# Performance work log

Hardware: AMD Instinct MI355X
Metric: run time of the kernel (lower is better)

## Reference

```python
import jax, jax.numpy as jnp
import numpy as np

B, S, A, E, H, V, P = 128, 256, 8, 300, 300, 50000, 3


def _gru(x, wih, whh, bih, bhh):
    """torch.nn.GRU (single layer, batch_first) with gate order r,z,n."""
    h0 = jnp.zeros((x.shape[0], whh.shape[1]), x.dtype)

    def step(h, xt):
        gi = xt @ wih.T + bih            # [B,3H]
        gh = h @ whh.T + bhh
        ir, iz, in_ = jnp.split(gi, 3, axis=-1)
        hr, hz, hn = jnp.split(gh, 3, axis=-1)
        r = jax.nn.sigmoid(ir + hr)
        z = jax.nn.sigmoid(iz + hz)
        n = jnp.tanh(in_ + r * hn)
        hnew = (1.0 - z) * n + z * h
        return hnew, hnew

    _, ys = jax.lax.scan(step, h0, jnp.swapaxes(x, 0, 1))  # scan over time
    return jnp.swapaxes(ys, 0, 1)                          # [B,S,H]


def setup_inputs() -> dict:
    key = jax.random.key(0)
    ks = jax.random.split(key, 16)
    rn = lambda k, shape, s=0.05: jax.random.normal(k, shape, jnp.float32) * s
    z = lambda *shape: jnp.zeros(shape, jnp.float32)
    return {
        "embed_table": rn(ks[0], (V, E), 1.0),
        "w1": rn(ks[1], (E, 3 * E)), "b1": z(E),
        "w2": rn(ks[2], (1, E)),
        "wm": rn(ks[3], (E, E)), "bm": z(E),
        "wd": rn(ks[4], (P, E)), "bd": z(P),
        "wih_l": rn(ks[5], (3 * H, E)), "whh_l": rn(ks[6], (3 * H, H)),
        "bih_l": z(3 * H), "bhh_l": z(3 * H),
        "wih_r": rn(ks[7], (3 * H, E)), "whh_r": rn(ks[8], (3 * H, H)),
        "bih_r": z(3 * H), "bhh_r": z(3 * H),
        "wml": rn(ks[9], (1, H)), "bml": z(1),
        "wmr": rn(ks[10], (1, H)), "bmr": z(1),
        # all token ids >= 1 so lengths are exactly the padded length (packing == identity)
        "text_raw_indices": jax.random.randint(ks[11], (B, S), 1, V),
        "aspect_indices": jax.random.randint(ks[12], (B, A), 1, V),
        "x_l": jax.random.randint(ks[13], (B, S), 1, V),
        "x_r": jax.random.randint(ks[14], (B, S), 1, V),
    }


def _forward(embed_table, w1, b1, w2, wm, bm, wd, bd,
             wih_l, whh_l, bih_l, bhh_l, wih_r, whh_r, bih_r, bhh_r,
             wml, bml, wmr, bmr, text, aspect, xl, xr):
    memory_len = jnp.sum(text != 0, -1)    # [B]
    aspect_len = jnp.sum(aspect != 0, -1)
    left_len = jnp.sum(xl != 0, -1)

    v_a = jnp.sum(embed_table[aspect], 1) / aspect_len[:, None].astype(jnp.float32)  # [B,E]
    memory = embed_table[text]             # [B,S,E]

    # ---- context attention (attention #1), fully vectorized ----
    ctx_l = _gru(embed_table[xl], wih_l, whh_l, bih_l, bhh_l)  # [B,S,H]
    ctx_r = _gru(embed_table[xr], wih_r, whh_r, bih_r, bhh_r)
    attn_l = jax.nn.sigmoid(jnp.einsum('bsh,h->bs', ctx_l, wml[0]) + bml[0]) + 0.5  # [B,S]
    attn_r = jax.nn.sigmoid(jnp.einsum('bsh,h->bs', ctx_r, wmr[0]) + bmr[0]) + 0.5

    idx = jnp.arange(S)[None, :]                      # [1,S]
    a_start = (left_len - aspect_len)[:, None]        # [B,1]
    a_end = left_len[:, None]
    # attn_r reversed over the first aspect_end positions: attn_rr[i,t] = attn_r[i, a_end-1-t]
    attn_rr = jnp.take_along_axis(attn_r, jnp.clip(a_end - 1 - idx, 0, S - 1), axis=1)
    # attn_l shifted by aspect_start: attn_ls[i,t] = attn_l[i, t - a_start]
    attn_ls = jnp.take_along_axis(attn_l, jnp.clip(idx - a_start, 0, S - 1), axis=1)
    w = jnp.where(idx < a_start, attn_rr,
                  jnp.where(idx < a_end, (attn_rr + attn_ls) * 0.5, attn_ls))
    w = jnp.where(idx < memory_len[:, None], w, 1.0)  # untouched past memory_len
    memory = memory * w[..., None]

    v_s = jnp.sum(memory, 1) / memory_len[:, None].astype(jnp.float32)  # [B,E]

    # ---- content attention (attention #2) ----
    feat = jnp.concatenate([memory,
                            jnp.broadcast_to(v_a[:, None, :], memory.shape),
                            jnp.broadcast_to(v_s[:, None, :], memory.shape)], -1)  # [B,S,3E]
    c = jnp.tanh(feat @ w1.T + b1) @ w2.T             # [B,S,1]
    alpha = jax.nn.softmax(c[..., 0], axis=1)         # [B,S]
    v_ts = jnp.einsum('bse,bs->be', memory, alpha)    # [B,E]

    v_ns = v_ts + v_s                                 # dropout is identity at eval
    v_ms = jnp.tanh(v_ns @ wm.T + bm)
    return jax.nn.softmax(v_ms @ wd.T + bd, axis=-1)  # [B,P]


def reference(embed_table, w1, b1, w2, wm, bm, wd, bd,
              wih_l, whh_l, bih_l, bhh_l, wih_r, whh_r, bih_r, bhh_r,
              wml, bml, wmr, bmr, text_raw_indices, aspect_indices, x_l, x_r):
    return _forward(embed_table, w1, b1, w2, wm, bm, wd, bd,
                    wih_l, whh_l, bih_l, bhh_l, wih_r, whh_r, bih_r, bhh_r,
                    wml, bml, wmr, bmr, text_raw_indices, aspect_indices, x_l, x_r)
```

## Files before the change

kernel.cpp:

```cpp
#include <hip/hip_runtime.h>
#include <hip/hip_bf16.h>
#include <math.h>

#define Bd 128
#define Sd 256
#define Ad 8
#define Ed 300
#define Hd 300
#define EP 320
#define Pd 3
#define UC 5
#define BG 8

typedef __attribute__((ext_vector_type(8))) short bfrag;
typedef __attribute__((ext_vector_type(4))) float f32x4;
typedef __attribute__((ext_vector_type(4))) int i32x4;

#define OFF_LENS   0u
#define OFF_FLAGS  4096u
#define OFF_VA     8192u
#define OFF_VS     172032u
#define OFF_U      335872u
#define OFF_ATTN   499712u
#define OFF_ALPHA  761856u
#define OFF_C      892928u
#define OFF_HF     1024000u
#define OFF_PART   1351680u
#define OFF_WF     11837440u
#define OFF_W1B    14295040u
#define OFF_XF     14499840u
#define OFF_MEMW   14499840u
#define WS_NEEDED  56442880u

__device__ __forceinline__ unsigned short f2bf(float f) {
    __hip_bfloat16 h = __float2bfloat16(f);
    return *reinterpret_cast<unsigned short*>(&h);
}
__device__ __forceinline__ float bf2f(unsigned short u) {
    __hip_bfloat16 h = *reinterpret_cast<__hip_bfloat16*>(&u);
    return __bfloat162float(h);
}
__device__ __forceinline__ float sigm(float x) {
    return __builtin_amdgcn_rcpf(1.f + __expf(-x));
}
__device__ __forceinline__ float fast_tanh(float x) {
    x = fminf(fmaxf(x, -15.f), 15.f);
    float e = __expf(2.f * x);
    return (e - 1.f) * __builtin_amdgcn_rcpf(e + 1.f);
}

__device__ __forceinline__ bfrag l2_load16b(const void* p) {
    bfrag v;
    asm volatile("global_load_dwordx4 %0, %1, off sc0"
                 : "=v"(v) : "v"(p) : "memory");
    return v;
}
__device__ __forceinline__ void l2_store16(void* p, i32x4 v) {
    asm volatile("global_store_dwordx4 %0, %1, off sc0"
                 :: "v"(p), "v"(v) : "memory");
}

__global__ void k_lengths(const int* __restrict__ text, const int* __restrict__ aspect,
                          const int* __restrict__ xl, int* __restrict__ lens) {
    int b = blockIdx.x;
    __shared__ int red[3];
    if (threadIdx.x < 3) red[threadIdx.x] = 0;
    __syncthreads();
    int t = threadIdx.x;
    if (t < Sd) {
        if (text[b*Sd + t] != 0) atomicAdd(&red[0], 1);
        if (xl[b*Sd + t]  != 0) atomicAdd(&red[2], 1);
    }
    if (t < Ad) { if (aspect[b*Ad + t] != 0) atomicAdd(&red[1], 1); }
    __syncthreads();
    if (t < 3) lens[b*4 + t] = red[t];
}

__global__ void k_va(const float* __restrict__ embed, const int* __restrict__ aspect,
                     const int* __restrict__ lens, float* __restrict__ va) {
    int b = blockIdx.x;
    __shared__ int aidx[Ad];
    if (threadIdx.x < Ad) aidx[threadIdx.x] = aspect[b*Ad + threadIdx.x];
    __syncthreads();
    float inv = 1.0f / (float)lens[b*4+1];
    for (int e = threadIdx.x; e < EP; e += blockDim.x) {
        float s = 0.f;
        if (e < Ed) {
            for (int a = 0; a < Ad; ++a) s += embed[(size_t)aidx[a]*Ed + e];
        }
        va[b*EP + e] = s * inv;
    }
}

__global__ void k_xf(const float* __restrict__ embed, const int* __restrict__ xl,
                     const int* __restrict__ xr, unsigned short* __restrict__ XF) {
    int side = blockIdx.x >> 8;
    int t = blockIdx.x & 255;
    const int* xs = side ? xr : xl;
    __shared__ int rows_s[Bd];
    if (threadIdx.x < Bd) rows_s[threadIdx.x] = xs[threadIdx.x*Sd + t];
    __syncthreads();
    unsigned short* dst = XF + ((size_t)(side*Sd + t))*40960;
    for (int idx = threadIdx.x; idx < 40960; idx += 256) {
        int bt = idx / 5120;
        int r1 = idx - bt*5120;
        int kt = r1 / 512;
        int r2 = r1 - kt*512;
        int lane = r2 >> 3, j = r2 & 7;
        int b = bt*16 + (lane & 15);
        int kk = kt*32 + (lane >> 4)*8 + j;
        float v = (kk < Ed) ? embed[(size_t)rows_s[b]*Ed + kk] : 0.f;
        dst[idx] = f2bf(v);
    }
}

__global__ void k_wfrag(const float* __restrict__ wih_l, const float* __restrict__ whh_l,
                        const float* __restrict__ wih_r, const float* __restrict__ whh_r,
                        unsigned short* __restrict__ WF) {
    int bid = blockIdx.x;
    int side = bid / 120;
    int r = bid - side*120;
    int mat = r / 60; r -= mat*60;
    int g = r / 20;
    int ut = r - g*20;
    const float* W = mat ? (side ? whh_r : whh_l) : (side ? wih_r : wih_l);
    unsigned short* dst = WF + (size_t)bid*5120;
    for (int idx = threadIdx.x; idx < 5120; idx += 256) {
        int kt = idx / 512;
        int r2 = idx - kt*512;
        int lane = r2 >> 3, j = r2 & 7;
        int unit = ut*16 + (lane & 15);
        int kk = kt*32 + (lane >> 4)*8 + j;
        float v = (unit < Hd && kk < Ed) ? W[(size_t)(g*Hd + unit)*Ed + kk] : 0.f;
        dst[idx] = f2bf(v);
    }
}

__global__ void k_w1conv(const float* __restrict__ w1, unsigned short* __restrict__ w1b) {
    int idx = blockIdx.x*256 + threadIdx.x;
    if (idx >= EP*EP) return;
    int e = idx / EP, k = idx - e*EP;
    float v = (e < Ed && k < Ed) ? w1[(size_t)e*900 + k] : 0.f;
    w1b[idx] = f2bf(v);
}

__global__ __launch_bounds__(256, 1) void k_gru(
        const unsigned short* __restrict__ WF,
        const unsigned short* __restrict__ XF,
        const float* __restrict__ bih_l, const float* __restrict__ bhh_l,
        const float* __restrict__ bih_r, const float* __restrict__ bhh_r,
        const float* __restrict__ wml, const float* __restrict__ wmr,
        unsigned short* __restrict__ HF,
        float* __restrict__ part, int* __restrict__ flags) {
    int bg = blockIdx.x & 7;
    int r8 = blockIdx.x >> 3;
    int side = r8 & 1;
    int uc = r8 >> 1;
    int tid = threadIdx.x;
    int w = tid >> 6, lane = tid & 63, ul = lane & 15, lq = lane >> 4;
    int utg = uc*4 + w;
    int u = utg*16 + ul;

    const float* bih = side ? bih_r : bih_l;
    const float* bhh = side ? bhh_r : bhh_l;
    const float* wmv = side ? wmr : wml;

    float bR=0.f, bZ=0.f, bNI=0.f, bNH=0.f, wml_r=0.f;
    if (u < Hd) {
        bR = bih[u] + bhh[u];
        bZ = bih[Hd+u] + bhh[Hd+u];
        bNI = bih[2*Hd+u];
        bNH = bhh[2*Hd+u];
        wml_r = wmv[u];
    }

    bfrag wI[3][10], wH[3][10];
    #pragma unroll
    for (int g = 0; g < 3; ++g) {
        const unsigned short* pI = WF + ((size_t)((side*2+0)*3+g)*20 + utg)*5120 + lane*8;
        const unsigned short* pH = WF + ((size_t)((side*2+1)*3+g)*20 + utg)*5120 + lane*8;
        #pragma unroll
        for (int kt = 0; kt < 10; ++kt) {
            wI[g][kt] = *(const bfrag*)(pI + kt*512);
            wH[g][kt] = *(const bfrag*)(pH + kt*512);
        }
    }

    __shared__ __align__(16) unsigned short hn_s[1024];
    int* flgL2 = flags + (side*8 + bg)*16;
    int* flgIC = flags + 512 + (side*8 + bg)*16;
    unsigned short* hfb = HF + (size_t)((side*8 + bg)*2)*5120;
    const unsigned short* xbase = XF + ((size_t)side*Sd*8 + bg)*5120 + lane*8;

    bfrag xA[10], xB[10];
    #pragma unroll
    for (int kt = 0; kt < 10; ++kt)
        xA[kt] = *(const bfrag*)(xbase + 0 + kt*512);

    float hreg[4] = {0.f,0.f,0.f,0.f};
    const f32x4 zero4 = {0.f,0.f,0.f,0.f};

#define GRU_STEP(T, XIN, XOUT) do {                                            \
    f32x4 aR = zero4, aZ = zero4, aNI = zero4, aNH = zero4;                    \
    _Pragma("unroll")                                                          \
    for (int kt = 0; kt < 10; ++kt) {                                          \
        aR  = __builtin_amdgcn_mfma_f32_16x16x32_bf16(XIN[kt], wI[0][kt], aR, 0,0,0); \
        aZ  = __builtin_amdgcn_mfma_f32_16x16x32_bf16(XIN[kt], wI[1][kt], aZ, 0,0,0); \
        aNI = __builtin_amdgcn_mfma_f32_16x16x32_bf16(XIN[kt], wI[2][kt], aNI, 0,0,0); \
    }                                                                          \
    if ((T) > 0) {                                                             \
        if (w == 0) {                                                          \
            int iters = 0;                                                     \
            while (true) {                                                     \
                int v = (T);                                                   \
                if (lane < UC)                                                 \
                    v = __hip_atomic_fetch_add(flgL2 + lane, 0, __ATOMIC_RELAXED, __HIP_MEMORY_SCOPE_WORKGROUP); \
                if (__all(v >= (T))) break;                                    \
                if (((++iters) & 63) == 0) {                                   \
                    int vv = (T);                                              \
                    if (lane < UC)                                             \
                        vv = __hip_atomic_load(flgIC + lane, __ATOMIC_RELAXED, __HIP_MEMORY_SCOPE_AGENT); \
                    if (__all(vv >= (T))) break;                               \
                }                                                              \
            }                                                                  \
        }                                                                      \
        __syncthreads();                                                       \
    }                                                                          \
    asm volatile("" ::: "memory");                                             \
    const unsigned short* hg = hfb + (size_t)((T) & 1)*5120 + lane*8;          \
    bfrag hf[10];                                                              \
    _Pragma("unroll")                                                          \
    for (int kt = 0; kt < 10; ++kt)                                            \
        hf[kt] = l2_load16b(hg + kt*512);                                      \
    asm volatile("s_waitcnt vmcnt(0)" ::: "memory");                           \
    __builtin_amdgcn_sched_barrier(0);                                         \
    _Pragma("unroll")                                                          \
    for (int kt = 0; kt < 10; ++kt) {                                          \
        aR  = __builtin_amdgcn_mfma_f32_16x16x32_bf16(hf[kt], wH[0][kt], aR, 0,0,0); \
        aZ  = __builtin_amdgcn_mfma_f32_16x16x32_bf16(hf[kt], wH[1][kt], aZ, 0,0,0); \
        aNH = __builtin_amdgcn_mfma_f32_16x16x32_bf16(hf[kt], wH[2][kt], aNH, 0,0,0); \
    }                                                                          \
    {                                                                          \
        int u_local = w*16 + ul;                                               \
        int kt_l = u_local >> 5, ko = u_local & 31;                            \
        _Pragma("unroll")                                                      \
        for (int i = 0; i < 4; ++i) {                                          \
            float rr = sigm(aR[i] + bR);                                       \
            float zz = sigm(aZ[i] + bZ);                                       \
            float nn = fast_tanh(aNI[i] + bNI + rr*(aNH[i] + bNH));            \
            float hv = (1.f - zz)*nn + zz*hreg[i];                             \
            hreg[i] = hv;                                                      \
            int rrow = lq*4 + i;                                               \
            hn_s[kt_l*512 + (rrow + ((ko>>3)<<4))*8 + (ko&7)] = f2bf(hv);      \
        }                                                                      \
    }                                                                          \
    __syncthreads();                                                           \
    {                                                                          \
        unsigned short* hd = hfb + (size_t)(((T)+1) & 1)*5120 + uc*1024;       \
        if (tid < 128)                                                         \
            l2_store16(hd + (size_t)tid*8, ((const i32x4*)hn_s)[tid]);         \
    }                                                                          \
    asm volatile("s_waitcnt vmcnt(0)" ::: "memory");                           \
    __syncthreads();                                                           \
    if ((T) < Sd-1 && tid == 0) {                                              \
        __hip_atomic_fetch_add(flgL2 + uc, 1, __ATOMIC_RELAXED, __HIP_MEMORY_SCOPE_WORKGROUP); \
        __hip_atomic_store(flgIC + uc, (T)+1, __ATOMIC_RELAXED, __HIP_MEMORY_SCOPE_AGENT); \
    }                                                                          \
    {                                                                          \
        int tn = ((T)+1 < Sd) ? (T)+1 : Sd-1;                                  \
        const unsigned short* xp = xbase + (size_t)tn*40960;                   \
        _Pragma("unroll")                                                      \
        for (int kt = 0; kt < 10; ++kt)                                        \
            XOUT[kt] = *(const bfrag*)(xp + kt*512);                           \
    }                                                                          \
    _Pragma("unroll")                                                          \
    for (int i = 0; i < 4; ++i) {                                              \
        float pv = hreg[i] * wml_r;                                            \
        pv += __shfl_xor(pv, 1, 64);                                           \
        pv += __shfl_xor(pv, 2, 64);                                           \
        pv += __shfl_xor(pv, 4, 64);                                           \
        pv += __shfl_xor(pv, 8, 64);                                           \
        if (ul == 0)                                                           \
            part[((size_t)((((side*8+bg)*UC + uc)*4 + w)*16) + lq*4 + i)*Sd + (T)] = pv; \
    }                                                                          \
} while (0)

    #pragma unroll 1
    for (int tt = 0; tt < Sd; tt += 2) {
        GRU_STEP(tt,   xA, xB);
        GRU_STEP(tt+1, xB, xA);
    }
#undef GRU_STEP
}

__global__ void k_attn(const float* __restrict__ part, const float* __restrict__ bml,
                       const float* __restrict__ bmr, float* __restrict__ attn) {
    int side = blockIdx.x >> 7;
    int b = blockIdx.x & 127;
    int bg = b >> 4, r = b & 15;
    int t = threadIdx.x;
    float s = 0.f;
    for (int c = 0; c < UC*4; ++c)
        s += part[((size_t)(((side*8+bg)*UC*4 + c)*16) + r)*Sd + t];
    float bias = side ? bmr[0] : bml[0];
    attn[(size_t)(side*Bd + b)*Sd + t] = sigm(s + bias) + 0.5f;
}

__global__ void k_wmem(const float* __restrict__ embed, const int* __restrict__ text,
                       const float* __restrict__ attn, const int* __restrict__ lens,
                       unsigned short* __restrict__ memw, float* __restrict__ vs) {
    int b = blockIdx.x;
    __shared__ float w_sh[Sd];
    __shared__ int text_s[Sd];
    int memlen = lens[b*4+0], asplen = lens[b*4+1], leftlen = lens[b*4+2];
    int a_start = leftlen - asplen, a_end = leftlen;
    const float* attl = attn + (size_t)b*Sd;
    const float* attr = attn + (size_t)(Bd + b)*Sd;
    if (threadIdx.x < Sd) {
        int i = threadIdx.x;
        int irr = a_end - 1 - i; irr = irr < 0 ? 0 : (irr > Sd-1 ? Sd-1 : irr);
        int ils = i - a_start;   ils = ils < 0 ? 0 : (ils > Sd-1 ? Sd-1 : ils);
        float arr_ = attr[irr], als = attl[ils];
        float w = (i < a_start) ? arr_ : ((i < a_end) ? 0.5f*(arr_+als) : als);
        if (i >= memlen) w = 1.0f;
        w_sh[i] = w;
        text_s[i] = text[b*Sd + i];
    }
    __syncthreads();
    int e = threadIdx.x;
    float acc = 0.f;
    float invm = 1.0f/(float)lens[b*4+0];
    for (int s = 0; s < Sd; ++s) {
        float v = (e < Ed) ? embed[(size_t)text_s[s]*Ed + e] : 0.f;
        float mw = v * w_sh[s];
        memw[((size_t)b*Sd + s)*EP + e] = f2bf(mw);
        acc += mw;
    }
    vs[b*EP + e] = acc * invm;
}

__global__ void k_u(const float* __restrict__ w1, const float* __restrict__ b1,
                    const float* __restrict__ va, const float* __restrict__ vs,
                    float* __restrict__ u) {
    int b = blockIdx.x;
    __shared__ float va_s[Ed], vs_s[Ed];
    for (int k = threadIdx.x; k < Ed; k += blockDim.x) {
        va_s[k] = va[b*EP+k];
        vs_s[k] = vs[b*EP+k];
    }
    __syncthreads();
    int e = threadIdx.x;
    if (e >= EP) return;
    float acc = 0.f;
    if (e < Ed) {
        acc = b1[e];
        const float* r = w1 + (size_t)e*900;
        for (int k = 0; k < Ed; ++k) acc += va_s[k]*r[300+k];
        for (int k = 0; k < Ed; ++k) acc += vs_s[k]*r[600+k];
    }
    u[b*EP + e] = acc;
}

__global__ __launch_bounds__(256) void k_c(const unsigned short* __restrict__ memw,
                   const unsigned short* __restrict__ w1b,
                   const float* __restrict__ u, const float* __restrict__ w2,
                   float* __restrict__ cout) {
    int b = blockIdx.x >> 2;
    int s0 = (blockIdx.x & 3) * 64;
    __shared__ __align__(16) unsigned short A_s[64*328];
    __shared__ __align__(16) unsigned short Bp_s[EP*32];
    __shared__ float u_s[EP], w2_s[EP];
    for (int i = threadIdx.x; i < EP; i += 256) {
        u_s[i] = u[b*EP + i];
        w2_s[i] = (i < Ed) ? w2[i] : 0.f;
    }
    const unsigned short* Ag = memw + ((size_t)b*Sd + s0)*EP;
    for (int c8 = threadIdx.x; c8 < 64*40; c8 += 256) {
        int r = c8 / 40, kk = (c8 - r*40)*8;
        *(bfrag*)(A_s + r*328 + kk) = *(const bfrag*)(Ag + (size_t)r*EP + kk);
    }

    int wave = threadIdx.x >> 6, lane = threadIdx.x & 63;
    int ul = lane & 15, lq = lane >> 4;
    const f32x4 zero4 = {0.f,0.f,0.f,0.f};
    f32x4 acc[20];
    #pragma unroll
    for (int n = 0; n < 20; ++n) acc[n] = zero4;

    for (int kp = 0; kp < 10; ++kp) {
        __syncthreads();
        for (int c8 = threadIdx.x; c8 < EP*4; c8 += 256) {
            int e = c8 >> 2, kk = (c8 & 3)*8;
            *(bfrag*)(Bp_s + e*32 + kk) = *(const bfrag*)(w1b + (size_t)e*EP + kp*32 + kk);
        }
        __syncthreads();
        bfrag a = *(const bfrag*)(A_s + (wave*16 + ul)*328 + kp*32 + lq*8);
        #pragma unroll
        for (int n = 0; n < 20; ++n) {
            bfrag bb = *(const bfrag*)(Bp_s + (n*16 + ul)*32 + lq*8);
            acc[n] = __builtin_amdgcn_mfma_f32_16x16x32_bf16(a, bb, acc[n], 0, 0, 0);
        }
    }
    float cs[4] = {0.f,0.f,0.f,0.f};
    #pragma unroll
    for (int n = 0; n < 20; ++n) {
        int e = n*16 + ul;
        #pragma unroll
        for (int i = 0; i < 4; ++i)
            cs[i] += w2_s[e] * fast_tanh(acc[n][i] + u_s[e]);
    }
    #pragma unroll
    for (int i = 0; i < 4; ++i) {
        float v = cs[i];
        v += __shfl_xor(v, 1, 64); v += __shfl_xor(v, 2, 64);
        v += __shfl_xor(v, 4, 64); v += __shfl_xor(v, 8, 64);
        if (ul == 0) cout[(size_t)b*Sd + s0 + wave*16 + lq*4 + i] = v;
    }
}

__global__ void k_alpha(const float* __restrict__ cin, float* __restrict__ alpha) {
    int b = blockIdx.x;
    int t = threadIdx.x;
    __shared__ float buf[Sd];
    float v = cin[(size_t)b*Sd + t];
    buf[t] = v; __syncthreads();
    for (int s2 = 128; s2 > 0; s2 >>= 1) {
        if (t < s2) buf[t] = fmaxf(buf[t], buf[t+s2]);
        __syncthreads();
    }
    float mx = buf[0];
    __syncthreads();
    float ex = __expf(v - mx);
    buf[t] = ex; __syncthreads();
    for (int s2 = 128; s2 > 0; s2 >>= 1) {
        if (t < s2) buf[t] += buf[t+s2];
        __syncthreads();
    }
    alpha[(size_t)b*Sd + t] = ex / buf[0];
}

__global__ void k_final(const unsigned short* __restrict__ memw, const float* __restrict__ alpha,
                        const float* __restrict__ vs, const float* __restrict__ wm,
                        const float* __restrict__ bm, const float* __restrict__ wd,
                        const float* __restrict__ bd, float* __restrict__ out) {
    int b = blockIdx.x;
    __shared__ float al_s[Sd];
    __shared__ float vns_s[Ed];
    __shared__ float vms_s[Ed];
    __shared__ float lg_s[Pd];
    if (threadIdx.x < Sd) al_s[threadIdx.x] = alpha[(size_t)b*Sd + threadIdx.x];
    __syncthreads();
    int e = threadIdx.x;
    if (e < Ed) {
        float acc = 0.f;
        const unsigned short* mp = memw + (size_t)b*Sd*EP + e;
        for (int s = 0; s < Sd; ++s) acc += bf2f(mp[(size_t)s*EP]) * al_s[s];
        vns_s[e] = acc + vs[b*EP + e];
    }
    __syncthreads();
    if (e < Ed) {
        float acc = bm[e];
        const float* r = wm + (size_t)e*Ed;
        for (int k = 0; k < Ed; ++k) acc += vns_s[k]*r[k];
        vms_s[e] = fast_tanh(acc);
    }
    __syncthreads();
    if (e < Pd) {
        float acc = bd[e];
        const float* r = wd + (size_t)e*Ed;
        for (int k = 0; k < Ed; ++k) acc += vms_s[k]*r[k];
        lg_s[e] = acc;
    }
    __syncthreads();
    if (e < Pd) {
        float m = fmaxf(lg_s[0], fmaxf(lg_s[1], lg_s[2]));
        float den = __expf(lg_s[0]-m)+__expf(lg_s[1]-m)+__expf(lg_s[2]-m);
        out[b*Pd + e] = __expf(lg_s[e]-m)/den;
    }
}

extern "C" void kernel_launch(void* const* d_in, const int* in_sizes, int n_in,
                              void* d_out, int out_size, void* d_ws, size_t ws_size,
                              hipStream_t stream) {
    const float* embed = (const float*)d_in[0];
    const float* w1    = (const float*)d_in[1];
    const float* b1    = (const float*)d_in[2];
    const float* w2    = (const float*)d_in[3];
    const float* wm    = (const float*)d_in[4];
    const float* bm    = (const float*)d_in[5];
    const float* wd    = (const float*)d_in[6];
    const float* bd    = (const float*)d_in[7];
    const float* wih_l = (const float*)d_in[8];
    const float* whh_l = (const float*)d_in[9];
    const float* bih_l = (const float*)d_in[10];
    const float* bhh_l = (const float*)d_in[11];
    const float* wih_r = (const float*)d_in[12];
    const float* whh_r = (const float*)d_in[13];
    const float* bih_r = (const float*)d_in[14];
    const float* bhh_r = (const float*)d_in[15];
    const float* wml   = (const float*)d_in[16];
    const float* bml   = (const float*)d_in[17];
    const float* wmr   = (const float*)d_in[18];
    const float* bmr   = (const float*)d_in[19];
    const int* text    = (const int*)d_in[20];
    const int* aspect  = (const int*)d_in[21];
    const int* xl      = (const int*)d_in[22];
    const int* xr      = (const int*)d_in[23];

    if (ws_size < (size_t)WS_NEEDED) return;
    char* ws = (char*)d_ws;
    int* lens            = (int*)(ws + OFF_LENS);
    int* flags           = (int*)(ws + OFF_FLAGS);
    float* va            = (float*)(ws + OFF_VA);
    float* vs            = (float*)(ws + OFF_VS);
    float* u             = (float*)(ws + OFF_U);
    float* attn          = (float*)(ws + OFF_ATTN);
    float* alpha         = (float*)(ws + OFF_ALPHA);
    float* c             = (float*)(ws + OFF_C);
    unsigned short* HF   = (unsigned short*)(ws + OFF_HF);
    float* part          = (float*)(ws + OFF_PART);
    unsigned short* WF   = (unsigned short*)(ws + OFF_WF);
    unsigned short* w1b  = (unsigned short*)(ws + OFF_W1B);
    unsigned short* XF   = (unsigned short*)(ws + OFF_XF);
    unsigned short* memw = (unsigned short*)(ws + OFF_MEMW);

    hipMemsetAsync(ws + OFF_FLAGS, 0, 4096, stream);
    hipMemsetAsync(ws + OFF_HF, 0, 327680, stream);

    k_lengths<<<128, 256, 0, stream>>>(text, aspect, xl, lens);
    k_va     <<<128, 320, 0, stream>>>(embed, aspect, lens, va);
    k_xf     <<<512, 256, 0, stream>>>(embed, xl, xr, XF);
    k_wfrag  <<<240, 256, 0, stream>>>(wih_l, whh_l, wih_r, whh_r, WF);
    k_w1conv <<<400, 256, 0, stream>>>(w1, w1b);
    k_gru    <<<80, 256, 0, stream>>>(WF, XF, bih_l, bhh_l, bih_r, bhh_r,
                                      wml, wmr, HF, part, flags);
    k_attn   <<<256, 256, 0, stream>>>(part, bml, bmr, attn);
    k_wmem   <<<128, 320, 0, stream>>>(embed, text, attn, lens, memw, vs);
    k_u      <<<128, 320, 0, stream>>>(w1, b1, va, vs, u);
    k_c      <<<512, 256, 0, stream>>>(memw, w1b, u, w2, c);
    k_alpha  <<<128, 256, 0, stream>>>(c, alpha);
    k_final  <<<128, 320, 0, stream>>>(memw, alpha, vs, wm, bm, wd, bd, (float*)d_out);
}
```

Baseline: 865.3 us.

## Vectorize bf16 packing kernels and split GRU step flags per wave

The xf and weight-fragment prep kernels now load 8 floats at once with vector loads and write 16-byte bf16 packs, replacing per-element scalar conversion. In the GRU recurrence, the two storing waves each publish their half of h and raise their own flag, so there are twice as many flags per unit chunk. This drops one block-wide barrier per timestep from the serial critical path. Pollers now check 2*UC flags, and the flag buffer must be large enough for the extra entries.

```diff
diff --git a/kernel.cpp b/kernel.cpp
--- a/kernel.cpp
+++ b/kernel.cpp
@@ -101,16 +101,28 @@
     if (threadIdx.x < Bd) rows_s[threadIdx.x] = xs[threadIdx.x*Sd + t];
     __syncthreads();
     unsigned short* dst = XF + ((size_t)(side*Sd + t))*40960;
-    for (int idx = threadIdx.x; idx < 40960; idx += 256) {
+    for (int v8 = threadIdx.x; v8 < 5120; v8 += 256) {
+        int idx = v8 << 3;
         int bt = idx / 5120;
         int r1 = idx - bt*5120;
-        int kt = r1 / 512;
-        int r2 = r1 - kt*512;
-        int lane = r2 >> 3, j = r2 & 7;
+        int kt = r1 >> 9;
+        int r2 = r1 & 511;
+        int lane = r2 >> 3;
         int b = bt*16 + (lane & 15);
-        int kk = kt*32 + (lane >> 4)*8 + j;
-        float v = (kk < Ed) ? embed[(size_t)rows_s[b]*Ed + kk] : 0.f;
-        dst[idx] = f2bf(v);
+        int kk = kt*32 + (lane >> 4)*8;
+        const float* src = embed + (size_t)rows_s[b]*Ed + kk;
+        unsigned short tmp[8];
+        if (kk + 8 <= Ed) {
+            f32x4 f0 = *(const f32x4*)(src);
+            f32x4 f1 = *(const f32x4*)(src + 4);
+            #pragma unroll
+            for (int j = 0; j < 4; ++j) { tmp[j] = f2bf(f0[j]); tmp[4+j] = f2bf(f1[j]); }
+        } else {
+            #pragma unroll
+            for (int j = 0; j < 8; ++j)
+                tmp[j] = (kk + j < Ed) ? f2bf(src[j]) : (unsigned short)0;
+        }
+        *(bfrag*)(dst + idx) = *(const bfrag*)tmp;
     }
 }
 
@@ -125,14 +137,28 @@
     int ut = r - g*20;
     const float* W = mat ? (side ? whh_r : whh_l) : (side ? wih_r : wih_l);
     unsigned short* dst = WF + (size_t)bid*5120;
-    for (int idx = threadIdx.x; idx < 5120; idx += 256) {
-        int kt = idx / 512;
-        int r2 = idx - kt*512;
-        int lane = r2 >> 3, j = r2 & 7;
+    for (int v8 = threadIdx.x; v8 < 640; v8 += 256) {
+        int idx = v8 << 3;
+        int kt = idx >> 9;
+        int r2 = idx & 511;
+        int lane = r2 >> 3;
         int unit = ut*16 + (lane & 15);
-        int kk = kt*32 + (lane >> 4)*8 + j;
-        float v = (unit < Hd && kk < Ed) ? W[(size_t)(g*Hd + unit)*Ed + kk] : 0.f;
-        dst[idx] = f2bf(v);
+        int kk = kt*32 + (lane >> 4)*8;
+        unsigned short tmp[8];
+        if (unit < Hd && kk + 8 <= Ed) {
+            const float* src = W + (size_t)(g*Hd + unit)*Ed + kk;
+            f32x4 f0 = *(const f32x4*)(src);
+            f32x4 f1 = *(const f32x4*)(src + 4);
+            #pragma unroll
+            for (int j = 0; j < 4; ++j) { tmp[j] = f2bf(f0[j]); tmp[4+j] = f2bf(f1[j]); }
+        } else {
+            #pragma unroll
+            for (int j = 0; j < 8; ++j) {
+                float v = (unit < Hd && kk + j < Ed) ? W[(size_t)(g*Hd + unit)*Ed + kk + j] : 0.f;
+                tmp[j] = f2bf(v);
+            }
+        }
+        *(bfrag*)(dst + idx) = *(const bfrag*)tmp;
     }
 }
 
@@ -213,12 +239,12 @@
             int iters = 0;                                                     \
             while (true) {                                                     \
                 int v = (T);                                                   \
-                if (lane < UC)                                                 \
+                if (lane < 2*UC)                                               \
                     v = __hip_atomic_fetch_add(flgL2 + lane, 0, __ATOMIC_RELAXED, __HIP_MEMORY_SCOPE_WORKGROUP); \
                 if (__all(v >= (T))) break;                                    \
                 if (((++iters) & 63) == 0) {                                   \
                     int vv = (T);                                              \
-                    if (lane < UC)                                             \
+                    if (lane < 2*UC)                                           \
                         vv = __hip_atomic_load(flgIC + lane, __ATOMIC_RELAXED, __HIP_MEMORY_SCOPE_AGENT); \
                     if (__all(vv >= (T))) break;                               \
                 }                                                              \
@@ -254,17 +280,15 @@
             hn_s[kt_l*512 + (rrow + ((ko>>3)<<4))*8 + (ko&7)] = f2bf(hv);      \
         }                                                                      \
     }                                                                          \
-    __syncthreads();                                                           \
-    {                                                                          \
+    __syncthreads();           \
+    if (w < 2) {                                                               \
         unsigned short* hd = hfb + (size_t)(((T)+1) & 1)*5120 + uc*1024;       \
-        if (tid < 128)                                                         \
-            l2_store16(hd + (size_t)tid*8, ((const i32x4*)hn_s)[tid]);         \
-    }                                                                          \
-    asm volatile("s_waitcnt vmcnt(0)" ::: "memory");                           \
-    __syncthreads();                                                           \
-    if ((T) < Sd-1 && tid == 0) {                                              \
-        __hip_atomic_fetch_add(flgL2 + uc, 1, __ATOMIC_RELAXED, __HIP_MEMORY_SCOPE_WORKGROUP); \
-        __hip_atomic_store(flgIC + uc, (T)+1, __ATOMIC_RELAXED, __HIP_MEMORY_SCOPE_AGENT); \
+        l2_store16(hd + (size_t)tid*8, ((const i32x4*)hn_s)[tid]);             \
+        asm volatile("s_waitcnt vmcnt(0)" ::: "memory");                       \
+        if (lane == 0 && (T) < Sd-1) {                                         \
+            __hip_atomic_fetch_add(flgL2 + uc*2 + w, 1, __ATOMIC_RELAXED, __HIP_MEMORY_SCOPE_WORKGROUP); \
+            __hip_atomic_store(flgIC + uc*2 + w, (T)+1, __ATOMIC_RELAXED, __HIP_MEMORY_SCOPE_AGENT); \
+        }                                                                      \
     }                                                                          \
     {                                                                          \
         int tn = ((T)+1 < Sd) ? (T)+1 : Sd-1;                                  \
```

Result: faster. 821.1 us, median of 2 (-5.1%).
